# Optimization experiments

Hardware: AMD Instinct MI355X
Metric: run time of the kernel (lower is better)

## Reference

```python
import jax, jax.numpy as jnp
import numpy as np

N_Q = 8  # number of residual quantization levels


def setup_inputs() -> dict:
    key = jax.random.key(0)
    k1, k2 = jax.random.split(key)
    hidden_states = jax.random.normal(k1, (8192, 128), dtype=jnp.float32)
    codebooks = jax.random.normal(k2, (N_Q, 256, 128), dtype=jnp.float32)
    return {"hidden_states": hidden_states, "codebooks": codebooks}


def reference(hidden_states, codebooks):
    """Residual VQ encode: per level, nearest codebook entry by L2, subtract, accumulate.

    hidden_states: [N, D]; codebooks: [n_q, bins, D].
    Returns (codes [n_q, N] int, quantized [N, D]).
    """
    residual = hidden_states
    quantized = jnp.zeros_like(hidden_states)
    codes = []
    for i in range(N_Q):  # small fixed loop over structurally distinct levels
        codebook = codebooks[i]  # [bins, D]
        # squared L2 distance, same math as the original broadcasted form
        dist = jnp.sum((residual[:, None, :] - codebook[None, :, :]) ** 2, axis=-1)  # [N, bins]
        idx = jnp.argmin(dist, axis=-1)  # [N]
        chosen = codebook[idx]  # [N, D]
        quantized = quantized + chosen
        residual = residual - chosen
        codes.append(idx)
    return jnp.stack(codes, axis=0), quantized
```

## Files before the change

kernel.cpp:

```cpp
#include <hip/hip_runtime.h>

#define NQ 8
#define BINS 256
#define D 128
#define RPB 32
#define THREADS 512
#define RSTRIDE 132
#define FREG 520

typedef short s8v __attribute__((ext_vector_type(8)));
typedef float f4v __attribute__((ext_vector_type(4)));

static __device__ __forceinline__ unsigned short bf16_rtne(float x) {
    unsigned u = __float_as_uint(x);
    unsigned r = (u + 0x7fffu + ((u >> 16) & 1u)) >> 16;
    return (unsigned short)r;
}
static __device__ __forceinline__ float bf16_to_f(unsigned short h) {
    return __uint_as_float(((unsigned)h) << 16);
}
struct Split3 { short h, m, l; };
static __device__ __forceinline__ Split3 split3(float x) {
    Split3 s;
    unsigned short hb = bf16_rtne(x);
    float r1 = x - bf16_to_f(hb);
    unsigned short mb = bf16_rtne(r1);
    unsigned short lb = bf16_rtne(r1 - bf16_to_f(mb));
    s.h = (short)hb; s.m = (short)mb; s.l = (short)lb;
    return s;
}
static __device__ __forceinline__ unsigned long long u64min(unsigned long long a, unsigned long long b) {
    return a < b ? a : b;
}
static __device__ __forceinline__ unsigned long long shfl_xor_u64(unsigned long long v, int mask) {
    int lo = (int)(unsigned)(v & 0xffffffffull);
    int hi = (int)(unsigned)(v >> 32);
    lo = __shfl_xor(lo, mask, 64);
    hi = __shfl_xor(hi, mask, 64);
    return ((unsigned long long)(unsigned)hi << 32) | (unsigned)lo;
}

__global__ __launch_bounds__(256) void rvq_prep(
    const float* __restrict__ cb, short* __restrict__ cb_hi,
    short* __restrict__ cb_mid, short* __restrict__ cb_lo,
    float* __restrict__ c2)
{
    __shared__ float st[16 * RSTRIDE];
    const int L = blockIdx.x >> 4;
    const int o = blockIdx.x & 15;
    const int t = threadIdx.x;

    const float4* src = (const float4*)(cb + ((size_t)L * BINS + o * 16) * D);
    #pragma unroll
    for (int i = 0; i < 2; ++i) {
        int f4 = i * 256 + t;
        int row = f4 >> 5, c4 = f4 & 31;
        float4 v = src[f4];
        float* d = &st[row * RSTRIDE + c4 * 4];
        d[0] = v.x; d[1] = v.y; d[2] = v.z; d[3] = v.w;
    }
    __syncthreads();

    const int bin = t >> 4;
    const int kc  = t & 15;
    const float* p = &st[bin * RSTRIDE + kc * 8];
    s8v h8, m8, l8;
    float s = 0.f;
    #pragma unroll
    for (int j = 0; j < 8; ++j) {
        float x = p[j];
        Split3 sp = split3(x);
        h8[j] = sp.h; m8[j] = sp.m; l8[j] = sp.l;
        s = fmaf(x, x, s);
    }
    int idx = (L * 16 + kc) * BINS + (o * 16 + bin);
    ((s8v*)cb_hi)[idx]  = h8;
    ((s8v*)cb_mid)[idx] = m8;
    ((s8v*)cb_lo)[idx]  = l8;
    s += __shfl_xor(s, 1, 64);
    s += __shfl_xor(s, 2, 64);
    s += __shfl_xor(s, 4, 64);
    s += __shfl_xor(s, 8, 64);
    if (kc == 0) c2[L * BINS + o * 16 + bin] = s;
}

static __device__ __forceinline__ void frag_store8(
    const float* rres, short* ah, short* am, short* al, int rr_, int g8)
{
    s8v h8, m8, l8;
    #pragma unroll
    for (int j = 0; j < 8; ++j) {
        Split3 sp = split3(rres[j]);
        h8[j] = sp.h; m8[j] = sp.m; l8[j] = sp.l;
    }
    int q = g8 & 3;
    int reg = (rr_ >> 4) * 4 + (g8 >> 2);
    int idx16 = q * 16 + (((rr_ & 15) + 4 * q) & 15);
    int off = reg * FREG + idx16 * 8;
    *(s8v*)&ah[off] = h8;
    *(s8v*)&am[off] = m8;
    *(s8v*)&al[off] = l8;
}

static __device__ __forceinline__ void issue_cb(
    int lv, int base16, int m, int quad,
    const s8v* __restrict__ bhp, const s8v* __restrict__ bmp, const s8v* __restrict__ blp,
    const float* __restrict__ c2p,
    s8v bh[4], s8v bm[4], s8v bl[4], f4v& c2v)
{
    const int bin = base16 + m;
    #pragma unroll
    for (int ks = 0; ks < 4; ++ks) {
        int idx = (lv * 16 + ks * 4 + quad) * BINS + bin;
        bh[ks] = bhp[idx];
        bm[ks] = bmp[idx];
        bl[ks] = blp[idx];
    }
    c2v = *(const f4v*)(c2p + lv * BINS + base16 + quad * 4);
}

static __device__ __forceinline__ unsigned long long cluster(
    const s8v bh[4], const s8v bm[4], const s8v bl[4],
    const s8v rfh[4], const s8v rfm[4], const s8v rfl[4],
    f4v c2c, int binbase, unsigned long long best)
{
    f4v a0 = {0.f, 0.f, 0.f, 0.f};
    f4v a1 = {0.f, 0.f, 0.f, 0.f};
    f4v a2 = {0.f, 0.f, 0.f, 0.f};
    __builtin_amdgcn_s_setprio(1);
    #pragma unroll
    for (int ks = 0; ks < 4; ++ks) {
        a0 = __builtin_amdgcn_mfma_f32_16x16x32_bf16(bh[ks], rfh[ks], a0, 0, 0, 0);
        a1 = __builtin_amdgcn_mfma_f32_16x16x32_bf16(bm[ks], rfh[ks], a1, 0, 0, 0);
        a1 = __builtin_amdgcn_mfma_f32_16x16x32_bf16(bh[ks], rfm[ks], a1, 0, 0, 0);
        a2 = __builtin_amdgcn_mfma_f32_16x16x32_bf16(bm[ks], rfm[ks], a2, 0, 0, 0);
        a2 = __builtin_amdgcn_mfma_f32_16x16x32_bf16(bl[ks], rfh[ks], a2, 0, 0, 0);
        a2 = __builtin_amdgcn_mfma_f32_16x16x32_bf16(bh[ks], rfl[ks], a2, 0, 0, 0);
    }
    __builtin_amdgcn_s_setprio(0);
    #pragma unroll
    for (int i = 0; i < 4; ++i) {
        float dot = a0[i] + (a1[i] + a2[i]);
        float k = fmaf(-2.f, dot, c2c[i]);
        unsigned u = __float_as_uint(k);
        u = (u & 0x80000000u) ? ~u : (u | 0x80000000u);
        best = u64min(best, ((unsigned long long)u << 32) | (unsigned)(binbase + i));
    }
    return best;
}

static __device__ __forceinline__ void load_afrag(
    const short* ah, const short* am, const short* al, int mt, int idx16,
    s8v rfh[4], s8v rfm[4], s8v rfl[4])
{
    #pragma unroll
    for (int ks = 0; ks < 4; ++ks) {
        int off = (mt * 4 + ks) * FREG + idx16 * 8;
        rfh[ks] = *(const s8v*)&ah[off];
        rfm[ks] = *(const s8v*)&am[off];
        rfl[ks] = *(const s8v*)&al[off];
    }
}

__global__ __launch_bounds__(THREADS, 2) void rvq_kernel(
    const float* __restrict__ hidden,
    const float* __restrict__ cb_f32,
    const short* __restrict__ cb_hi,
    const short* __restrict__ cb_mid,
    const short* __restrict__ cb_lo,
    const float* __restrict__ c2p,
    float* __restrict__ out_codes,
    float* __restrict__ out_quant,
    int N)
{
    __shared__ __align__(16) short ah[8 * FREG];
    __shared__ __align__(16) short am[8 * FREG];
    __shared__ __align__(16) short al[8 * FREG];
    __shared__ __align__(16) unsigned long long redw[RPB][10];

    const int t = threadIdx.x;
    const int w = t >> 6;
    const int l = t & 63;
    const int quad = l >> 4;
    const int m = l & 15;
    const int woff = w * 32;
    const int row0 = blockIdx.x * RPB;
    const int rr_ = t >> 4;
    const int g8  = t & 15;
    const int dbase = g8 * 8;

    float rres[8], hreg[8];
    {
        const f4v* hp = (const f4v*)(hidden + (size_t)(row0 + rr_) * D + dbase);
        f4v v0 = hp[0], v1 = hp[1];
        #pragma unroll
        for (int j = 0; j < 4; ++j) { hreg[j] = v0[j]; hreg[4 + j] = v1[j]; }
        #pragma unroll
        for (int j = 0; j < 8; ++j) rres[j] = hreg[j];
    }
    frag_store8(rres, ah, am, al, rr_, g8);

    const s8v* bhp = (const s8v*)cb_hi;
    const s8v* bmp = (const s8v*)cb_mid;
    const s8v* blp = (const s8v*)cb_lo;

    s8v bh0[4], bm0[4], bl0[4];
    s8v bh1[4], bm1[4], bl1[4];
    f4v c20, c21;
    issue_cb(0, woff, m, quad, bhp, bmp, blp, c2p, bh0, bm0, bl0, c20);

    const int idx16 = quad * 16 + ((m + 4 * quad) & 15);

    for (int level = 0; level < NQ; ++level) {
        __syncthreads();

        issue_cb(level, woff + 16, m, quad, bhp, bmp, blp, c2p, bh1, bm1, bl1, c21);

        unsigned long long best0 = ~0ull, best1 = ~0ull;
        s8v rfh[4], rfm[4], rfl[4];

        load_afrag(ah, am, al, 0, idx16, rfh, rfm, rfl);
        best0 = cluster(bh0, bm0, bl0, rfh, rfm, rfl, c20, woff + quad * 4, best0);
        best0 = cluster(bh1, bm1, bl1, rfh, rfm, rfl, c21, woff + 16 + quad * 4, best0);

        load_afrag(ah, am, al, 1, idx16, rfh, rfm, rfl);
        best1 = cluster(bh0, bm0, bl0, rfh, rfm, rfl, c20, woff + quad * 4, best1);
        if (level + 1 < NQ)
            issue_cb(level + 1, woff, m, quad, bhp, bmp, blp, c2p, bh0, bm0, bl0, c20);
        best1 = cluster(bh1, bm1, bl1, rfh, rfm, rfl, c21, woff + 16 + quad * 4, best1);

        best0 = u64min(best0, shfl_xor_u64(best0, 16));
        best0 = u64min(best0, shfl_xor_u64(best0, 32));
        best1 = u64min(best1, shfl_xor_u64(best1, 16));
        best1 = u64min(best1, shfl_xor_u64(best1, 32));
        if (l < 16) {
            redw[m][w]      = best0;
            redw[16 + m][w] = best1;
        }
        __syncthreads();

        unsigned long long mn;
        {
            const ulonglong2* rp = (const ulonglong2*)&redw[rr_][0];
            ulonglong2 p0 = rp[0], p1 = rp[1], p2 = rp[2], p3 = rp[3];
            mn = u64min(u64min(u64min(p0.x, p0.y), u64min(p1.x, p1.y)),
                        u64min(u64min(p2.x, p2.y), u64min(p3.x, p3.y)));
        }
        const int wb = (int)(mn & 0xffffffffull);
        if (g8 == 0)
            out_codes[(size_t)level * N + row0 + rr_] = (float)wb;

        {
            const f4v* cp = (const f4v*)(cb_f32 + ((size_t)level * BINS + wb) * D + dbase);
            f4v c0 = cp[0], c1 = cp[1];
            #pragma unroll
            for (int j = 0; j < 4; ++j) { rres[j] -= c0[j]; rres[4 + j] -= c1[j]; }
        }
        if (level + 1 < NQ)
            frag_store8(rres, ah, am, al, rr_, g8);
    }

    {
        f4v q0, q1;
        #pragma unroll
        for (int j = 0; j < 4; ++j) {
            q0[j] = hreg[j] - rres[j];
            q1[j] = hreg[4 + j] - rres[4 + j];
        }
        f4v* op = (f4v*)(out_quant + (size_t)(row0 + rr_) * D + dbase);
        op[0] = q0; op[1] = q1;
    }
}

extern "C" void kernel_launch(void* const* d_in, const int* in_sizes, int n_in,
                              void* d_out, int out_size, void* d_ws, size_t ws_size,
                              hipStream_t stream) {
    const float* hidden    = (const float*)d_in[0];
    const float* codebooks = (const float*)d_in[1];
    float* out = (float*)d_out;
    const int N = in_sizes[0] / D;
    float* out_codes = out;
    float* out_quant = out + (size_t)NQ * N;

    char* ws = (char*)d_ws;
    short* cb_hi  = (short*)ws;
    short* cb_mid = (short*)(ws +  512 * 1024);
    short* cb_lo  = (short*)(ws + 1024 * 1024);
    float* c2     = (float*)(ws + 1536 * 1024);

    rvq_prep<<<dim3(NQ * 16), 256, 0, stream>>>(codebooks, cb_hi, cb_mid, cb_lo, c2);
    rvq_kernel<<<dim3(N / RPB), THREADS, 0, stream>>>(
        hidden, codebooks, cb_hi, cb_mid, cb_lo, c2, out_codes, out_quant, N);
}
```

Baseline: 102.5 us.

## Prefetch both codebook halves a level ahead and use lighter barriers

Result: slower. 104.8 us (+2.2%).

```diff
diff --git a/kernel.cpp b/kernel.cpp
--- a/kernel.cpp
+++ b/kernel.cpp
@@ -9,7 +9,10 @@
 #define FREG 520
 
 typedef short s8v __attribute__((ext_vector_type(8)));
+typedef short s4v __attribute__((ext_vector_type(4)));
 typedef float f4v __attribute__((ext_vector_type(4)));
+
+#define BAR_LGKM() asm volatile("s_waitcnt lgkmcnt(0)\n\ts_barrier" ::: "memory")
 
 static __device__ __forceinline__ unsigned short bf16_rtne(float x) {
     unsigned u = __float_as_uint(x);
@@ -84,22 +87,24 @@
     if (kc == 0) c2[L * BINS + o * 16 + bin] = s;
 }
 
-static __device__ __forceinline__ void frag_store8(
-    const float* rres, short* ah, short* am, short* al, int rr_, int g8)
-{
-    s8v h8, m8, l8;
-    #pragma unroll
-    for (int j = 0; j < 8; ++j) {
+static __device__ __forceinline__ void frag_store4(
+    const float* rres, short* ah, short* am, short* al, int rr_, int g8, int half)
+{
+    s4v h4, m4, l4;
+    #pragma unroll
+    for (int j = 0; j < 4; ++j) {
         Split3 sp = split3(rres[j]);
-        h8[j] = sp.h; m8[j] = sp.m; l8[j] = sp.l;
-    }
-    int q = g8 & 3;
-    int reg = (rr_ >> 4) * 4 + (g8 >> 2);
-    int idx16 = q * 16 + (((rr_ & 15) + 4 * q) & 15);
-    int off = reg * FREG + idx16 * 8;
-    *(s8v*)&ah[off] = h8;
-    *(s8v*)&am[off] = m8;
-    *(s8v*)&al[off] = l8;
+        h4[j] = sp.h; m4[j] = sp.m; l4[j] = sp.l;
+    }
+    int q  = g8 & 3;
+    int ks = g8 >> 2;
+    int mt = rr_ >> 4;
+    int r16 = rr_ & 15;
+    int idx16 = q * 16 + ((r16 + 4 * q) & 15);
+    int off = (mt * 4 + ks) * FREG + idx16 * 8 + half * 4;
+    *(s4v*)&ah[off] = h4;
+    *(s4v*)&am[off] = m4;
+    *(s4v*)&al[off] = l4;
 }
 
 static __device__ __forceinline__ void issue_cb(
@@ -162,7 +167,9 @@
     }
 }
 
-__global__ __launch_bounds__(THREADS, 2) void rvq_kernel(
+__global__ __launch_bounds__(THREADS)
+__attribute__((amdgpu_waves_per_eu(2, 2)))
+void rvq_kernel(
     const float* __restrict__ hidden,
     const float* __restrict__ cb_f32,
     const short* __restrict__ cb_hi,
@@ -198,7 +205,8 @@
         #pragma unroll
         for (int j = 0; j < 8; ++j) rres[j] = hreg[j];
     }
-    frag_store8(rres, ah, am, al, rr_, g8);
+    frag_store4(rres,     ah, am, al, rr_, g8, 0);
+    frag_store4(rres + 4, ah, am, al, rr_, g8, 1);
 
     const s8v* bhp = (const s8v*)cb_hi;
     const s8v* bmp = (const s8v*)cb_mid;
@@ -207,14 +215,13 @@
     s8v bh0[4], bm0[4], bl0[4];
     s8v bh1[4], bm1[4], bl1[4];
     f4v c20, c21;
-    issue_cb(0, woff, m, quad, bhp, bmp, blp, c2p, bh0, bm0, bl0, c20);
+    issue_cb(0, woff,      m, quad, bhp, bmp, blp, c2p, bh0, bm0, bl0, c20);
+    issue_cb(0, woff + 16, m, quad, bhp, bmp, blp, c2p, bh1, bm1, bl1, c21);
 
     const int idx16 = quad * 16 + ((m + 4 * quad) & 15);
 
     for (int level = 0; level < NQ; ++level) {
-        __syncthreads();
-
-        issue_cb(level, woff + 16, m, quad, bhp, bmp, blp, c2p, bh1, bm1, bl1, c21);
+        BAR_LGKM();
 
         unsigned long long best0 = ~0ull, best1 = ~0ull;
         s8v rfh[4], rfm[4], rfl[4];
@@ -228,6 +235,8 @@
         if (level + 1 < NQ)
             issue_cb(level + 1, woff, m, quad, bhp, bmp, blp, c2p, bh0, bm0, bl0, c20);
         best1 = cluster(bh1, bm1, bl1, rfh, rfm, rfl, c21, woff + 16 + quad * 4, best1);
+        if (level + 1 < NQ)
+            issue_cb(level + 1, woff + 16, m, quad, bhp, bmp, blp, c2p, bh1, bm1, bl1, c21);
 
         best0 = u64min(best0, shfl_xor_u64(best0, 16));
         best0 = u64min(best0, shfl_xor_u64(best0, 32));
@@ -237,7 +246,7 @@
             redw[m][w]      = best0;
             redw[16 + m][w] = best1;
         }
-        __syncthreads();
+        BAR_LGKM();
 
         unsigned long long mn;
         {
@@ -256,8 +265,10 @@
             #pragma unroll
             for (int j = 0; j < 4; ++j) { rres[j] -= c0[j]; rres[4 + j] -= c1[j]; }
         }
-        if (level + 1 < NQ)
-            frag_store8(rres, ah, am, al, rr_, g8);
+        if (level + 1 < NQ) {
+            frag_store4(rres,     ah, am, al, rr_, g8, 0);
+            frag_store4(rres + 4, ah, am, al, rr_, g8, 1);
+        }
     }
 
     {
```
